# Optimization experiments

Hardware: AMD Instinct MI355X
Metric: run time of the kernel (lower is better)

## Reference

```python
import jax, jax.numpy as jnp
import numpy as np
import math


def setup_inputs() -> dict:
    key = jax.random.key(0)
    ks = jax.random.split(key, 8)
    B, S, dim = 4, 1024, 2048
    H, D = 16, 128          # n_heads = dim // core_dim
    T = 1024                # cached kv length
    w_scale = 1.0 / math.sqrt(dim)
    return {
        "x": jax.random.normal(ks[0], (B, S, dim), dtype=jnp.float32),
        "k_cache": jax.random.normal(ks[1], (B, H, T, D), dtype=jnp.float32),
        "v_cache": jax.random.normal(ks[2], (B, H, T, D), dtype=jnp.float32),
        "Wq": jax.random.normal(ks[3], (dim, dim), dtype=jnp.float32) * w_scale,
        "bq": jnp.zeros((dim,), jnp.float32),
        "Wk": jax.random.normal(ks[4], (dim, dim), dtype=jnp.float32) * w_scale,
        "bk": jnp.zeros((dim,), jnp.float32),
        "Wv": jax.random.normal(ks[5], (dim, dim), dtype=jnp.float32) * w_scale,
        "bv": jnp.zeros((dim,), jnp.float32),
        "Wo": jax.random.normal(ks[6], (dim, dim), dtype=jnp.float32) * w_scale,
        "bo": jnp.zeros((dim,), jnp.float32),
    }


def _split_heads(t, H):
    # [B, S, dim] -> [B, H, S, D]
    B, S, dim = t.shape
    return t.reshape(B, S, H, dim // H).transpose(0, 2, 1, 3)


def reference(x, k_cache, v_cache, Wq, bq, Wk, bk, Wv, bv, Wo, bo):
    B, S, dim = x.shape
    H = k_cache.shape[1]
    D = dim // H
    T = k_cache.shape[2]

    q = _split_heads(x @ Wq.T + bq, H)                 # [B,H,S,D]
    k_new = _split_heads(x @ Wk.T + bk, H)             # [B,H,S,D]
    v_new = _split_heads(x @ Wv.T + bv, H)

    k = jnp.concatenate([k_cache, k_new], axis=2)      # [B,H,T+S,D]
    v = jnp.concatenate([v_cache, v_new], axis=2)

    scale = 1.0 / math.sqrt(D)
    scores = jnp.einsum("bhqd,bhkd->bhqk", q, k) * scale   # [B,H,S,T+S]

    # causal mask with cache offset: query i may attend to key j iff j <= i + T
    q_pos = jnp.arange(S)[:, None] + T
    k_pos = jnp.arange(T + S)[None, :]
    mask = k_pos <= q_pos                              # [S, T+S]
    scores = jnp.where(mask[None, None], scores, jnp.finfo(scores.dtype).min)

    attn = jax.nn.softmax(scores, axis=-1)
    ctx = jnp.einsum("bhqk,bhkd->bhqd", attn, v)       # [B,H,S,D]
    ctx = ctx.transpose(0, 2, 1, 3).reshape(B, S, dim) # merge heads

    out = ctx @ Wo.T + bo                              # dropout is identity (p=0 / eval)
    return (out, k, v)
```

## Files before the change

kernel.cpp:

```cpp
#include <hip/hip_runtime.h>
#include <hip/hip_bf16.h>

typedef float f32x4 __attribute__((ext_vector_type(4)));
typedef __bf16 bf16x8 __attribute__((ext_vector_type(8)));
typedef unsigned short u16x8 __attribute__((ext_vector_type(8)));

#define DIMK 2048
#define QSCALE ((float)(0.08838834764831845 * 1.4426950408889634))

__device__ __forceinline__ unsigned short f2bf(float f) {
    union { float f; unsigned int u; } v; v.f = f;
    unsigned int r = v.u + 0x7fffu + ((v.u >> 16) & 1u);
    return (unsigned short)(r >> 16);
}
__device__ __forceinline__ float bf2f(unsigned short u) {
    union { unsigned int i; float f; } v; v.i = ((unsigned int)u) << 16; return v.f;
}

__device__ __forceinline__ void lds_load16(void* lds, const void* gsrc) {
    __builtin_amdgcn_global_load_lds(
        (const __attribute__((address_space(1))) unsigned int*)gsrc,
        (__attribute__((address_space(3))) unsigned int*)lds,
        16, 0, 0);
}

__global__ __launch_bounds__(256) void prep_all(
    const float* __restrict__ x,  const float* __restrict__ Wq,
    const float* __restrict__ Wk, const float* __restrict__ Wv,
    const float* __restrict__ Wo,
    const float* __restrict__ kc, const float* __restrict__ vc,
    unsigned short* __restrict__ xbf, unsigned short* __restrict__ Wqb,
    unsigned short* __restrict__ Wkb, unsigned short* __restrict__ Wvb,
    unsigned short* __restrict__ Wob,
    float* __restrict__ kout, unsigned short* __restrict__ Kbf,
    float* __restrict__ vout, unsigned short* __restrict__ Vtb)
{
    const int bid = blockIdx.x;
    const int tid = threadIdx.x;

    if (bid < 24576) {
        int i = bid * 256 + tid;
        const float* src; unsigned short* dst; size_t off;
        if (i < 2097152) { src = x; dst = xbf; off = i; }
        else {
            int j = (i - 2097152) >> 20;
            off = (size_t)((i - 2097152) & 1048575);
            src = j == 0 ? Wq : j == 1 ? Wk : j == 2 ? Wv : Wo;
            dst = j == 0 ? Wqb : j == 1 ? Wkb : j == 2 ? Wvb : Wob;
        }
        f32x4 v = *(const f32x4*)(src + off * 4);
        ushort4 pk = { f2bf(v[0]), f2bf(v[1]), f2bf(v[2]), f2bf(v[3]) };
        *(ushort4*)(dst + off * 4) = pk;
    } else if (bid < 32768) {
        size_t i4 = (size_t)(bid - 24576) * 256 + tid;
        size_t e = i4 * 4;
        size_t bh = e >> 17, rem = e & 131071;
        f32x4 v = *(const f32x4*)(kc + e);
        size_t dsto = (bh << 18) + rem;
        *(f32x4*)(kout + dsto) = v;
        ushort4 pk = { f2bf(v[0]), f2bf(v[1]), f2bf(v[2]), f2bf(v[3]) };
        *(ushort4*)(Kbf + dsto) = pk;
    } else {
        __shared__ unsigned short T[128 * 72];
        const int o = bid - 32768;
        const int kv0 = (o & 15) * 64;
        const int bh = o >> 4;
        const float* src = vc + ((size_t)bh << 17) + (size_t)kv0 * 128;
        float* vdst = vout + ((size_t)bh << 18) + (size_t)kv0 * 128;
        #pragma unroll
        for (int r = 0; r < 8; ++r) {
            int e4 = r * 256 + tid;
            int kv = e4 >> 5, d0 = (e4 & 31) << 2;
            f32x4 v = *(const f32x4*)(src + kv * 128 + d0);
            *(f32x4*)(vdst + kv * 128 + d0) = v;
            #pragma unroll
            for (int i = 0; i < 4; ++i) T[(d0 + i) * 72 + kv] = f2bf(v[i]);
        }
        __syncthreads();
        #pragma unroll
        for (int r = 0; r < 8; ++r) {
            int e = r * 256 + tid;
            int d = e >> 4, k4 = (e & 15) << 2;
            ushort4 pk = { T[d * 72 + k4], T[d * 72 + k4 + 1], T[d * 72 + k4 + 2], T[d * 72 + k4 + 3] };
            *(ushort4*)(Vtb + ((size_t)bh * 128 + d) * 2048 + kv0 + k4) = pk;
        }
    }
}

__device__ __forceinline__ void gemm_core(
    const unsigned short* __restrict__ A16, const unsigned short* __restrict__ W16,
    int m0, int n0, int tid, int w, int g, int c, int wr, int wc,
    unsigned short* As, unsigned short* Bs, f32x4 (&acc)[4][4])
{
    const int arow = tid >> 2;
    const int acol = (tid & 3) << 3;
    const unsigned short* Arow0 = A16 + (size_t)(m0 + arow) * DIMK + acol;
    const unsigned short* Arow1 = A16 + (size_t)(m0 + 64 + arow) * DIMK + acol;
    const unsigned short* Wrow0 = W16 + (size_t)(n0 + arow) * DIMK + acol;
    const unsigned short* Wrow1 = W16 + (size_t)(n0 + 64 + arow) * DIMK + acol;
    unsigned short* AsB0 = &As[(w * 64) * 8];
    unsigned short* AsB1 = &As[(256 + w * 64) * 8];
    unsigned short* BsB0 = &Bs[(w * 64) * 8];
    unsigned short* BsB1 = &Bs[(256 + w * 64) * 8];

    for (int k0 = 0; k0 < DIMK; k0 += 32) {
        __syncthreads();
        lds_load16(AsB0, Arow0 + k0);
        lds_load16(AsB1, Arow1 + k0);
        lds_load16(BsB0, Wrow0 + k0);
        lds_load16(BsB1, Wrow1 + k0);
        __syncthreads();

        bf16x8 af[4], bfr[4];
        #pragma unroll
        for (int i = 0; i < 4; ++i)
            af[i] = *(const bf16x8*)(&As[(wr * 64 + i * 16 + c) * 32 + g * 8]);
        #pragma unroll
        for (int i = 0; i < 4; ++i)
            bfr[i] = *(const bf16x8*)(&Bs[(wc * 64 + i * 16 + c) * 32 + g * 8]);
        #pragma unroll
        for (int i = 0; i < 4; ++i)
            #pragma unroll
            for (int j = 0; j < 4; ++j)
                acc[i][j] = __builtin_amdgcn_mfma_f32_16x16x32_bf16(af[i], bfr[j], acc[i][j], 0, 0, 0);
    }
}

__global__ __launch_bounds__(256) void gemm_qkv(
    const unsigned short* __restrict__ xbf,
    const unsigned short* __restrict__ Wqb, const unsigned short* __restrict__ Wkb,
    const unsigned short* __restrict__ Wvb,
    const float* __restrict__ bq, const float* __restrict__ bk, const float* __restrict__ bv,
    unsigned short* __restrict__ Qbf,
    float* __restrict__ kout, unsigned short* __restrict__ Kbf,
    float* __restrict__ vout, unsigned short* __restrict__ Vtb)
{
    const int o = blockIdx.x;
    const int xcd = o & 7;
    const int k = o >> 3;
    const int mblk = k & 31;
    const int nloc = k >> 5;
    const int nblk = xcd * 6 + nloc;
    const int m0 = mblk * 128;
    const int n0g = nblk * 128;
    const int mi = n0g >> 11;
    const int n0 = n0g & 2047;

    const unsigned short* W16 = mi == 0 ? Wqb : (mi == 1 ? Wkb : Wvb);
    const float* bias = mi == 0 ? bq : (mi == 1 ? bk : bv);

    const int tid = threadIdx.x;
    const int lane = tid & 63;
    const int w = tid >> 6;
    const int g = lane >> 4;
    const int c = lane & 15;
    const int wr = w >> 1, wc = w & 1;

    __shared__ unsigned short As[128 * 32];
    __shared__ unsigned short Bs[128 * 32];

    f32x4 acc[4][4];
    #pragma unroll
    for (int i = 0; i < 4; ++i)
        #pragma unroll
        for (int j = 0; j < 4; ++j)
            acc[i][j] = f32x4{0.f, 0.f, 0.f, 0.f};

    gemm_core(xbf, W16, m0, n0, tid, w, g, c, wr, wc, As, Bs, acc);

    #pragma unroll
    for (int j = 0; j < 4; ++j) {
        const int n = n0 + wc * 64 + j * 16 + c;
        const float bn = bias[n];
        const int hh = n >> 7, d = n & 127;
        #pragma unroll
        for (int i = 0; i < 4; ++i) {
            float y4[4];
            #pragma unroll
            for (int tq = 0; tq < 4; ++tq) y4[tq] = acc[i][j][tq] + bn;
            const int mb = m0 + wr * 64 + i * 16 + g * 4;
            if (mi == 0) {
                #pragma unroll
                for (int tq = 0; tq < 4; ++tq) {
                    int m = mb + tq; int b = m >> 10, s = m & 1023;
                    Qbf[((((size_t)b * 16 + hh) << 10) + s) * 128 + d] = f2bf(y4[tq] * QSCALE);
                }
            } else if (mi == 1) {
                #pragma unroll
                for (int tq = 0; tq < 4; ++tq) {
                    int m = mb + tq; int b = m >> 10, s = m & 1023;
                    kout[(((size_t)b * 16 + hh) * 2048 + 1024 + s) * 128 + d] = y4[tq];
                    Kbf[(((size_t)b * 16 + hh) << 18) + (size_t)(1024 + s) * 128 + d] = f2bf(y4[tq]);
                }
            } else {
                #pragma unroll
                for (int tq = 0; tq < 4; ++tq) {
                    int m = mb + tq; int b = m >> 10, s = m & 1023;
                    vout[(((size_t)b * 16 + hh) * 2048 + 1024 + s) * 128 + d] = y4[tq];
                }
                int b = mb >> 10, s = mb & 1023;
                ushort4 pk = { f2bf(y4[0]), f2bf(y4[1]), f2bf(y4[2]), f2bf(y4[3]) };
                *(ushort4*)(Vtb + (((size_t)b * 16 + hh) * 128 + d) * 2048 + 1024 + s) = pk;
            }
        }
    }
}

__global__ __launch_bounds__(256) void gemm_wo(
    const unsigned short* __restrict__ ctx, const unsigned short* __restrict__ Wob,
    const float* __restrict__ bo, float* __restrict__ outp)
{
    const int o = blockIdx.x;
    const int xcd = o & 7;
    const int k = o >> 3;
    const int mblk = k & 31;
    const int nloc = k >> 5;
    const int nblk = xcd * 2 + nloc;
    const int m0 = mblk * 128;
    const int n0 = nblk * 128;

    const int tid = threadIdx.x;
    const int lane = tid & 63;
    const int w = tid >> 6;
    const int g = lane >> 4;
    const int c = lane & 15;
    const int wr = w >> 1, wc = w & 1;

    __shared__ unsigned short As[128 * 32];
    __shared__ unsigned short Bs[128 * 32];

    f32x4 acc[4][4];
    #pragma unroll
    for (int i = 0; i < 4; ++i)
        #pragma unroll
        for (int j = 0; j < 4; ++j)
            acc[i][j] = f32x4{0.f, 0.f, 0.f, 0.f};

    gemm_core(ctx, Wob, m0, n0, tid, w, g, c, wr, wc, As, Bs, acc);

    #pragma unroll
    for (int j = 0; j < 4; ++j) {
        const int n = n0 + wc * 64 + j * 16 + c;
        const float bn = bo[n];
        #pragma unroll
        for (int i = 0; i < 4; ++i) {
            const int mb = m0 + wr * 64 + i * 16 + g * 4;
            #pragma unroll
            for (int tq = 0; tq < 4; ++tq)
                outp[(size_t)(mb + tq) * 2048 + n] = acc[i][j][tq] + bn;
        }
    }
}

__global__ __launch_bounds__(256) void attn8(
    const unsigned short* __restrict__ Qbf,
    const unsigned short* __restrict__ Kbf,
    const unsigned short* __restrict__ Vtb,
    unsigned short* __restrict__ Pp,
    float* __restrict__ Mp,
    float* __restrict__ Lp)
{
    const int o = blockIdx.x;
    const int xcd = o & 7;
    const int kk0 = o >> 3;
    const int half = kk0 & 1;
    const int qt = 7 - ((kk0 >> 1) & 7);
    const int bh = (kk0 >> 4) * 8 + xcd;

    const int tid = threadIdx.x;
    const int lane = tid & 63;
    const int w = tid >> 6;
    const int g = lane >> 4;
    const int c = lane & 15;
    const int cswz = (c & 7) << 3;

    __shared__ unsigned short Ks[2][64 * 128];
    __shared__ unsigned short Vs[128 * 64];

    const unsigned short* Qb = Qbf + ((size_t)bh * 1024 + qt * 128) * 128;
    const unsigned short* Kb = Kbf + ((size_t)bh << 18);
    const unsigned short* Vt = Vtb + ((size_t)bh << 18);

    bf16x8 aq[2][4];
    #pragma unroll
    for (int m2 = 0; m2 < 2; ++m2)
        #pragma unroll
        for (int kd = 0; kd < 4; ++kd)
            aq[m2][kd] = *(const bf16x8*)(Qb + (w * 32 + m2 * 16 + c) * 128 + kd * 32 + g * 8);

    f32x4 od[2][8];
    #pragma unroll
    for (int m2 = 0; m2 < 2; ++m2)
        #pragma unroll
        for (int nf = 0; nf < 8; ++nf)
            od[m2][nf] = f32x4{0.f, 0.f, 0.f, 0.f};
    float mrow[2] = { -1e30f, -1e30f };
    float lrow[2] = { 0.f, 0.f };

    const int krow = tid >> 4;
    const int kswz = (((tid & 15) << 4) ^ ((krow & 7) << 4)) >> 1;
    const unsigned short* Kl = Kb + (size_t)krow * 128 + kswz;

    const int vd = tid >> 3;
    const int ck = tid & 7;
    const int kkv = ck >> 2;
    const int av = (ck >> 1) & 1;
    const int p0 = kkv * 32 + (((2 * ck) & 3) << 3) + av * 4;
    const int p1 = kkv * 32 + (((2 * ck + 1) & 3) << 3) + av * 4;

    const int cnt = 9 + qt;
    const int t0 = half * cnt;
    const int lim_min = 1024 + qt * 128 + w * 32;

    u16x8 vreg0, vreg1, vreg2, vreg3;

    {
        const int kv0 = t0 * 64;
        #pragma unroll
        for (int r = 0; r < 4; ++r)
            lds_load16(&Ks[0][w * 512 + r * 2048], Kl + (size_t)(kv0 + r * 16) * 128);
        vreg0 = *(const u16x8*)(Vt + (size_t)(vd +  0) * 2048 + kv0 + ck * 8);
        vreg1 = *(const u16x8*)(Vt + (size_t)(vd + 32) * 2048 + kv0 + ck * 8);
        vreg2 = *(const u16x8*)(Vt + (size_t)(vd + 64) * 2048 + kv0 + ck * 8);
        vreg3 = *(const u16x8*)(Vt + (size_t)(vd + 96) * 2048 + kv0 + ck * 8);
        #pragma unroll
        for (int r = 0; r < 4; ++r) {
            const int d = vd + r * 32;
            const int sw = (d & 7) << 3;
            unsigned short* row = &Vs[d * 64];
            u16x8 vv = r == 0 ? vreg0 : r == 1 ? vreg1 : r == 2 ? vreg2 : vreg3;
            ushort4 lo = { vv[0], vv[1], vv[2], vv[3] };
            ushort4 hi = { vv[4], vv[5], vv[6], vv[7] };
            *(ushort4*)(&row[p0 ^ sw]) = lo;
            *(ushort4*)(&row[p1 ^ sw]) = hi;
        }
        __syncthreads();
    }

    int cur = 0;
    for (int t = t0; t < t0 + cnt; ++t) {
        const int kv0 = t * 64;
        const bool next = (t + 1 < t0 + cnt);

        if (next) {
            const int kvn = kv0 + 64;
            #pragma unroll
            for (int r = 0; r < 4; ++r)
                lds_load16(&Ks[cur ^ 1][w * 512 + r * 2048], Kl + (size_t)(kvn + r * 16) * 128);
            vreg0 = *(const u16x8*)(Vt + (size_t)(vd +  0) * 2048 + kvn + ck * 8);
            vreg1 = *(const u16x8*)(Vt + (size_t)(vd + 32) * 2048 + kvn + ck * 8);
            vreg2 = *(const u16x8*)(Vt + (size_t)(vd + 64) * 2048 + kvn + ck * 8);
            vreg3 = *(const u16x8*)(Vt + (size_t)(vd + 96) * 2048 + kvn + ck * 8);
        }

        const unsigned short* Ksc = &Ks[cur][0];

        f32x4 sc[2][4];
        #pragma unroll
        for (int m2 = 0; m2 < 2; ++m2)
            #pragma unroll
            for (int n = 0; n < 4; ++n)
                sc[m2][n] = f32x4{0.f, 0.f, 0.f, 0.f};
        #pragma unroll
        for (int kd = 0; kd < 4; ++kd) {
            bf16x8 bk[4];
            #pragma unroll
            for (int n = 0; n < 4; ++n)
                bk[n] = *(const bf16x8*)(&Ksc[(n * 16 + c) * 128 + ((kd * 32 + g * 8) ^ cswz)]);
            #pragma unroll
            for (int m2 = 0; m2 < 2; ++m2)
                #pragma unroll
                for (int n = 0; n < 4; ++n)
                    sc[m2][n] = __builtin_amdgcn_mfma_f32_16x16x32_bf16(bk[n], aq[m2][kd], sc[m2][n], 0, 0, 0);
        }

        const bool need_mask = (kv0 + 63 > lim_min);
        #pragma unroll
        for (int m2 = 0; m2 < 2; ++m2) {
            if (need_mask) {
                const int lim = lim_min + m2 * 16 + c;
                #pragma unroll
                for (int n = 0; n < 4; ++n)
                    #pragma unroll
                    for (int j = 0; j < 4; ++j)
                        if (kv0 + n * 16 + g * 4 + j > lim) sc[m2][n][j] = -1e30f;
            }
            float t4[4];
            #pragma unroll
            for (int n = 0; n < 4; ++n)
                t4[n] = fmaxf(fmaxf(sc[m2][n][0], sc[m2][n][1]),
                              fmaxf(sc[m2][n][2], sc[m2][n][3]));
            float rmax = fmaxf(fmaxf(t4[0], t4[1]), fmaxf(t4[2], t4[3]));
            rmax = fmaxf(rmax, __shfl_xor(rmax, 16));
            rmax = fmaxf(rmax, __shfl_xor(rmax, 32));

            if (!__all(rmax <= mrow[m2] + 8.0f)) {
                const float mnew = fmaxf(mrow[m2], rmax);
                const float fs = exp2f(mrow[m2] - mnew);
                mrow[m2] = mnew;
                lrow[m2] *= fs;
                #pragma unroll
                for (int j = 0; j < 4; ++j) {
                    const float fsj = __shfl(fs, (lane & 48) | (g * 4 + j));
                    #pragma unroll
                    for (int nf = 0; nf < 8; ++nf)
                        od[m2][nf][j] *= fsj;
                }
            }
            const float mm = mrow[m2];
            float s4[4];
            #pragma unroll
            for (int n = 0; n < 4; ++n) {
                #pragma unroll
                for (int j = 0; j < 4; ++j) {
                    float p = exp2f(sc[m2][n][j] - mm);
                    sc[m2][n][j] = p;
                }
                s4[n] = (sc[m2][n][0] + sc[m2][n][1]) + (sc[m2][n][2] + sc[m2][n][3]);
            }
            float rsum = (s4[0] + s4[1]) + (s4[2] + s4[3]);
            rsum += __shfl_xor(rsum, 16);
            rsum += __shfl_xor(rsum, 32);
            lrow[m2] += rsum;
        }

        bf16x8 pa[2][2];
        #pragma unroll
        for (int m2 = 0; m2 < 2; ++m2)
            #pragma unroll
            for (int kk = 0; kk < 2; ++kk)
                #pragma unroll
                for (int e = 0; e < 8; ++e)
                    pa[m2][kk][e] = (__bf16)sc[m2][2 * kk + (e >> 2)][e & 3];

        #pragma unroll
        for (int kk = 0; kk < 2; ++kk) {
            #pragma unroll
            for (int nf = 0; nf < 8; ++nf) {
                bf16x8 bv = *(const bf16x8*)(&Vs[(nf * 16 + c) * 64 + ((kk * 32 + g * 8) ^ cswz)]);
                od[0][nf] = __builtin_amdgcn_mfma_f32_16x16x32_bf16(pa[0][kk], bv, od[0][nf], 0, 0, 0);
                od[1][nf] = __builtin_amdgcn_mfma_f32_16x16x32_bf16(pa[1][kk], bv, od[1][nf], 0, 0, 0);
            }
        }

        __syncthreads();

        if (next) {
            #pragma unroll
            for (int r = 0; r < 4; ++r) {
                const int d = vd + r * 32;
                const int sw = (d & 7) << 3;
                unsigned short* row = &Vs[d * 64];
                u16x8 vv = r == 0 ? vreg0 : r == 1 ? vreg1 : r == 2 ? vreg2 : vreg3;
                ushort4 lo = { vv[0], vv[1], vv[2], vv[3] };
                ushort4 hi = { vv[4], vv[5], vv[6], vv[7] };
                *(ushort4*)(&row[p0 ^ sw]) = lo;
                *(ushort4*)(&row[p1 ^ sw]) = hi;
            }
        }

        __syncthreads();
        cur ^= 1;
    }

    const size_t pbase = ((size_t)(half * 64 + bh) * 1024 + qt * 128) * 128;
    const int mlbase = (half * 64 + bh) * 1024 + qt * 128;
    if (lane < 16) {
        #pragma unroll
        for (int m2 = 0; m2 < 2; ++m2) {
            Mp[mlbase + w * 32 + m2 * 16 + c] = mrow[m2];
            Lp[mlbase + w * 32 + m2 * 16 + c] = lrow[m2];
        }
    }
    #pragma unroll
    for (int m2 = 0; m2 < 2; ++m2) {
        #pragma unroll
        for (int j = 0; j < 4; ++j) {
            const float lj = __shfl(lrow[m2], (lane & 48) | (g * 4 + j));
            const float rl = 1.0f / lj;
            const int ql = w * 32 + m2 * 16 + g * 4 + j;
            #pragma unroll
            for (int nf = 0; nf < 8; ++nf)
                Pp[pbase + (size_t)ql * 128 + nf * 16 + c] = f2bf(od[m2][nf][j] * rl);
        }
    }
}

__global__ __launch_bounds__(256) void merge_ctx(
    const unsigned short* __restrict__ Pp, const float* __restrict__ Mp,
    const float* __restrict__ Lp, unsigned short* __restrict__ ctx)
{
    const int idx = blockIdx.x * 256 + threadIdx.x;
    const int r = idx >> 4;
    const int dc = (idx & 15) << 3;
    const float m0 = Mp[r], m1 = Mp[65536 + r];
    const float l0 = Lp[r], l1 = Lp[65536 + r];
    const float M = fmaxf(m0, m1);
    float w0 = l0 * exp2f(m0 - M);
    float w1 = l1 * exp2f(m1 - M);
    const float inv = 1.0f / (w0 + w1);
    w0 *= inv; w1 *= inv;
    u16x8 a = *(const u16x8*)(Pp + (size_t)r * 128 + dc);
    u16x8 bb = *(const u16x8*)(Pp + (size_t)8388608 + (size_t)r * 128 + dc);
    const int bh = r >> 10, q = r & 1023;
    unsigned short* dst = ctx + ((size_t)(bh >> 4) * 1024 + q) * 2048 + (bh & 15) * 128 + dc;
    u16x8 outv;
    #pragma unroll
    for (int e = 0; e < 8; ++e)
        outv[e] = f2bf(w0 * bf2f(a[e]) + w1 * bf2f(bb[e]));
    *(u16x8*)dst = outv;
}

__global__ __launch_bounds__(256) void copy_cache(
    const float* __restrict__ kc, const float* __restrict__ vc,
    float* __restrict__ kout, float* __restrict__ vout)
{
    size_t i4 = (size_t)blockIdx.x * 256 + threadIdx.x;
    const float* src = blockIdx.y ? vc : kc;
    float* dst = blockIdx.y ? vout : kout;
    size_t e = i4 * 4;
    size_t bh = e >> 17, rem = e & 131071;
    f32x4 v = *(const f32x4*)(src + e);
    *(f32x4*)(dst + (bh << 18) + rem) = v;
}

template<int MODE, bool ABF16>
__global__ __launch_bounds__(256) void gemm_bt(
    const void* __restrict__ Ag, const float* __restrict__ Wf,
    const float* __restrict__ bias, void* __restrict__ dst)
{
    const int tid = threadIdx.x;
    const int lane = tid & 63;
    const int w = tid >> 6;
    const int g = lane >> 4;
    const int c = lane & 15;
    const int wr = w >> 1, wc = w & 1;
    const int m0 = blockIdx.y * 128;
    const int n0 = blockIdx.x * 128;

    __shared__ unsigned short As[128 * 40];
    __shared__ unsigned short Bs[128 * 40];

    f32x4 acc[4][4];
    #pragma unroll
    for (int i = 0; i < 4; ++i)
        #pragma unroll
        for (int j = 0; j < 4; ++j)
            acc[i][j] = f32x4{0.f, 0.f, 0.f, 0.f};

    for (int k0 = 0; k0 < DIMK; k0 += 32) {
        __syncthreads();
        if constexpr (ABF16) {
            const unsigned short* A16 = (const unsigned short*)Ag;
            #pragma unroll
            for (int r = 0; r < 2; ++r) {
                int e8 = r * 256 + tid;
                int row = e8 >> 2, col = (e8 & 3) << 3;
                *(uint4*)(&As[row * 40 + col]) =
                    *(const uint4*)(A16 + (size_t)(m0 + row) * DIMK + k0 + col);
            }
        } else {
            const float* Af = (const float*)Ag;
            #pragma unroll
            for (int r = 0; r < 4; ++r) {
                int e4 = r * 256 + tid;
                int row = e4 >> 3, col = (e4 & 7) << 2;
                f32x4 v = *(const f32x4*)(Af + (size_t)(m0 + row) * DIMK + k0 + col);
                ushort4 pk = { f2bf(v[0]), f2bf(v[1]), f2bf(v[2]), f2bf(v[3]) };
                *(ushort4*)(&As[row * 40 + col]) = pk;
            }
        }
        {
            #pragma unroll
            for (int r = 0; r < 4; ++r) {
                int e4 = r * 256 + tid;
                int row = e4 >> 3, col = (e4 & 7) << 2;
                f32x4 v = *(const f32x4*)(Wf + (size_t)(n0 + row) * DIMK + k0 + col);
                ushort4 pk = { f2bf(v[0]), f2bf(v[1]), f2bf(v[2]), f2bf(v[3]) };
                *(ushort4*)(&Bs[row * 40 + col]) = pk;
            }
        }
        __syncthreads();

        bf16x8 af[4], bfr[4];
        #pragma unroll
        for (int i = 0; i < 4; ++i)
            af[i] = *(const bf16x8*)(&As[(wr * 64 + i * 16 + c) * 40 + g * 8]);
        #pragma unroll
        for (int i = 0; i < 4; ++i)
            bfr[i] = *(const bf16x8*)(&Bs[(wc * 64 + i * 16 + c) * 40 + g * 8]);
        #pragma unroll
        for (int i = 0; i < 4; ++i)
            #pragma unroll
            for (int j = 0; j < 4; ++j)
                acc[i][j] = __builtin_amdgcn_mfma_f32_16x16x32_bf16(af[i], bfr[j], acc[i][j], 0, 0, 0);
    }

    #pragma unroll
    for (int j = 0; j < 4; ++j) {
        const int n = n0 + wc * 64 + j * 16 + c;
        const float bn = bias[n];
        #pragma unroll
        for (int i = 0; i < 4; ++i) {
            float y4[4];
            #pragma unroll
            for (int tq = 0; tq < 4; ++tq) y4[tq] = acc[i][j][tq] + bn;
            const int mb = m0 + wr * 64 + i * 16 + g * 4;
            if constexpr (MODE == 0) {
                #pragma unroll
                for (int tq = 0; tq < 4; ++tq) {
                    int m = mb + tq; int b = m >> 10, s = m & 1023;
                    int hh = n >> 7, d = n & 127;
                    ((unsigned short*)dst)[((((size_t)b * 16 + hh) << 10) + s) * 128 + d] = f2bf(y4[tq] * QSCALE);
                }
            } else if constexpr (MODE == 1) {
                #pragma unroll
                for (int tq = 0; tq < 4; ++tq) {
                    int m = mb + tq; int b = m >> 10, s = m & 1023;
                    int hh = n >> 7, d = n & 127;
                    ((float*)dst)[(((size_t)b * 16 + hh) * 2048 + 1024 + s) * 128 + d] = y4[tq];
                }
            } else {
                #pragma unroll
                for (int tq = 0; tq < 4; ++tq)
                    ((float*)dst)[(size_t)(mb + tq) * 2048 + n] = y4[tq];
            }
        }
    }
}

__global__ __launch_bounds__(256) void attn_stage(
    const unsigned short* __restrict__ Qbf,
    const float* __restrict__ Kf, const float* __restrict__ Vf,
    unsigned short* __restrict__ ctx)
{
    const int qt = blockIdx.x;
    const int bh = blockIdx.y;
    const int b = bh >> 4, h = bh & 15;
    const int tid = threadIdx.x;
    const int lane = tid & 63;
    const int w = tid >> 6;
    const int g = lane >> 4;
    const int c = lane & 15;

    __shared__ unsigned short Ksl[64 * 136];
    __shared__ unsigned short Vtl[128 * 72];
    __shared__ unsigned short Ps[4 * 32 * 72];

    bf16x8 aq[2][4];
    const unsigned short* Qb = Qbf + ((size_t)bh * 1024 + qt * 128) * 128;
    #pragma unroll
    for (int m2 = 0; m2 < 2; ++m2)
        #pragma unroll
        for (int kk = 0; kk < 4; ++kk)
            aq[m2][kk] = *(const bf16x8*)(Qb + (w * 32 + m2 * 16 + c) * 128 + kk * 32 + g * 8);

    f32x4 od[2][8];
    #pragma unroll
    for (int m2 = 0; m2 < 2; ++m2)
        #pragma unroll
        for (int nf = 0; nf < 8; ++nf)
            od[m2][nf] = f32x4{0.f, 0.f, 0.f, 0.f};
    float mrow[2][4], lrow[2][4];
    #pragma unroll
    for (int m2 = 0; m2 < 2; ++m2)
        #pragma unroll
        for (int j = 0; j < 4; ++j) { mrow[m2][j] = -1e30f; lrow[m2][j] = 0.f; }

    const float* Kb = Kf + (size_t)bh * 2048 * 128;
    const float* Vb = Vf + (size_t)bh * 2048 * 128;
    const int ntiles = 18 + 2 * qt;

    for (int t = 0; t < ntiles; ++t) {
        __syncthreads();
        const float* Kt = Kb + (size_t)t * 64 * 128;
        #pragma unroll
        for (int r = 0; r < 8; ++r) {
            int e4 = r * 256 + tid;
            int kv = e4 >> 5, d0 = (e4 & 31) << 2;
            f32x4 v = *(const f32x4*)(Kt + kv * 128 + d0);
            ushort4 pk = { f2bf(v[0]), f2bf(v[1]), f2bf(v[2]), f2bf(v[3]) };
            *(ushort4*)(&Ksl[kv * 136 + d0]) = pk;
        }
        const float* Vg = Vb + (size_t)t * 64 * 128;
        #pragma unroll
        for (int r = 0; r < 8; ++r) {
            int e4 = tid * 8 + r;
            int kv = e4 >> 5, d0 = (e4 & 31) << 2;
            f32x4 v = *(const f32x4*)(Vg + kv * 128 + d0);
            #pragma unroll
            for (int i = 0; i < 4; ++i)
                Vtl[(d0 + i) * 72 + kv] = f2bf(v[i]);
        }
        __syncthreads();

        f32x4 sc[2][4];
        #pragma unroll
        for (int m2 = 0; m2 < 2; ++m2)
            #pragma unroll
            for (int n = 0; n < 4; ++n)
                sc[m2][n] = f32x4{0.f, 0.f, 0.f, 0.f};
        #pragma unroll
        for (int kk = 0; kk < 4; ++kk) {
            bf16x8 bk[4];
            #pragma unroll
            for (int n = 0; n < 4; ++n)
                bk[n] = *(const bf16x8*)(&Ksl[(n * 16 + c) * 136 + kk * 32 + g * 8]);
            #pragma unroll
            for (int m2 = 0; m2 < 2; ++m2)
                #pragma unroll
                for (int n = 0; n < 4; ++n)
                    sc[m2][n] = __builtin_amdgcn_mfma_f32_16x16x32_bf16(aq[m2][kk], bk[n], sc[m2][n], 0, 0, 0);
        }

        const int kvbase = t * 64;
        #pragma unroll
        for (int m2 = 0; m2 < 2; ++m2) {
            #pragma unroll
            for (int j = 0; j < 4; ++j) {
                const int qg = qt * 128 + w * 32 + m2 * 16 + g * 4 + j;
                const int lim = qg + 1024;
                float rmax = -1e30f;
                #pragma unroll
                for (int n = 0; n < 4; ++n) {
                    float s = sc[m2][n][j] * QSCALE;
                    if (kvbase + n * 16 + c > lim) s = -1e30f;
                    sc[m2][n][j] = s;
                    rmax = fmaxf(rmax, s);
                }
                #pragma unroll
                for (int off = 1; off < 16; off <<= 1)
                    rmax = fmaxf(rmax, __shfl_xor(rmax, off));
                float mold = mrow[m2][j];
                float mnew = fmaxf(mold, rmax);
                mrow[m2][j] = mnew;
                float fs = exp2f(mold - mnew);
                float rsum = 0.f;
                #pragma unroll
                for (int n = 0; n < 4; ++n) {
                    float p = exp2f(sc[m2][n][j] - mnew);
                    sc[m2][n][j] = p;
                    rsum += p;
                }
                #pragma unroll
                for (int off = 1; off < 16; off <<= 1)
                    rsum += __shfl_xor(rsum, off);
                lrow[m2][j] = lrow[m2][j] * fs + rsum;
                #pragma unroll
                for (int nf = 0; nf < 8; ++nf)
                    od[m2][nf][j] *= fs;
            }
        }

        unsigned short* Pw = &Ps[w * 32 * 72];
        #pragma unroll
        for (int m2 = 0; m2 < 2; ++m2)
            #pragma unroll
            for (int n = 0; n < 4; ++n)
                #pragma unroll
                for (int j = 0; j < 4; ++j)
                    Pw[(m2 * 16 + g * 4 + j) * 72 + n * 16 + c] = f2bf(sc[m2][n][j]);

        #pragma unroll
        for (int kk = 0; kk < 2; ++kk) {
            bf16x8 ap0 = *(const bf16x8*)(&Ps[(w * 32 + c) * 72 + kk * 32 + g * 8]);
            bf16x8 ap1 = *(const bf16x8*)(&Ps[(w * 32 + 16 + c) * 72 + kk * 32 + g * 8]);
            #pragma unroll
            for (int nf = 0; nf < 8; ++nf) {
                bf16x8 bv = *(const bf16x8*)(&Vtl[(nf * 16 + c) * 72 + kk * 32 + g * 8]);
                od[0][nf] = __builtin_amdgcn_mfma_f32_16x16x32_bf16(ap0, bv, od[0][nf], 0, 0, 0);
                od[1][nf] = __builtin_amdgcn_mfma_f32_16x16x32_bf16(ap1, bv, od[1][nf], 0, 0, 0);
            }
        }
    }

    #pragma unroll
    for (int m2 = 0; m2 < 2; ++m2) {
        #pragma unroll
        for (int j = 0; j < 4; ++j) {
            const int qg = qt * 128 + w * 32 + m2 * 16 + g * 4 + j;
            const float rl = 1.0f / lrow[m2][j];
            #pragma unroll
            for (int nf = 0; nf < 8; ++nf) {
                const int d = nf * 16 + c;
                ctx[((size_t)b * 1024 + qg) * 2048 + h * 128 + d] = f2bf(od[m2][nf][j] * rl);
            }
        }
    }
}

extern "C" void kernel_launch(void* const* d_in, const int* in_sizes, int n_in,
                              void* d_out, int out_size, void* d_ws, size_t ws_size,
                              hipStream_t stream) {
    const float* x  = (const float*)d_in[0];
    const float* kc = (const float*)d_in[1];
    const float* vc = (const float*)d_in[2];
    const float* Wq = (const float*)d_in[3];
    const float* bq = (const float*)d_in[4];
    const float* Wk = (const float*)d_in[5];
    const float* bk = (const float*)d_in[6];
    const float* Wv = (const float*)d_in[7];
    const float* bv = (const float*)d_in[8];
    const float* Wo = (const float*)d_in[9];
    const float* bo = (const float*)d_in[10];

    float* outp = (float*)d_out;
    float* kout = outp + (size_t)8388608;
    float* vout = outp + (size_t)25165824;

    unsigned short* Qbf = (unsigned short*)d_ws;
    unsigned short* ctx = Qbf + (size_t)8388608;
    unsigned short* Kbf = ctx + (size_t)8388608;
    unsigned short* Vtb = Kbf + (size_t)16777216;
    unsigned short* xbf = Vtb + (size_t)16777216;
    unsigned short* Wqb = xbf + (size_t)8388608;
    unsigned short* Wkb = Wqb + (size_t)4194304;
    unsigned short* Wvb = Wkb + (size_t)4194304;
    unsigned short* Wob = Wvb + (size_t)4194304;
    unsigned short* Pp = xbf;
    float* Mp = (float*)Wvb;
    float* Lp = Mp + (size_t)131072;

    const bool full = ws_size >= (size_t)150994944;

    if (full) {
        prep_all<<<33792, 256, 0, stream>>>(x, Wq, Wk, Wv, Wo, kc, vc,
                                            xbf, Wqb, Wkb, Wvb, Wob,
                                            kout, Kbf, vout, Vtb);
        gemm_qkv<<<1536, 256, 0, stream>>>(xbf, Wqb, Wkb, Wvb, bq, bk, bv,
                                           Qbf, kout, Kbf, vout, Vtb);
        attn8<<<1024, 256, 0, stream>>>(Qbf, Kbf, Vtb, Pp, Mp, Lp);
        merge_ctx<<<4096, 256, 0, stream>>>(Pp, Mp, Lp, ctx);
        gemm_wo<<<512, 256, 0, stream>>>(ctx, Wob, bo, outp);
    } else {
        copy_cache<<<dim3(8192, 2), 256, 0, stream>>>(kc, vc, kout, vout);
        gemm_bt<0, false><<<dim3(16, 32), 256, 0, stream>>>(x, Wq, bq, Qbf);
        gemm_bt<1, false><<<dim3(16, 32), 256, 0, stream>>>(x, Wk, bk, kout);
        gemm_bt<1, false><<<dim3(16, 32), 256, 0, stream>>>(x, Wv, bv, vout);
        attn_stage<<<dim3(8, 64), 256, 0, stream>>>(Qbf, kout, vout, ctx);
        gemm_bt<2, true><<<dim3(16, 32), 256, 0, stream>>>(ctx, Wo, bo, outp);
    }
}
```

Before: 435.4 us.

## Pre-tile and pre-swizzle V^T so attention loads it directly into LDS with 8 waves

The producers of V^T (prep_all and gemm_qkv) now write it as 64-key tiles that already carry the LDS permutation and XOR swizzle. The attention kernel can then copy V into a double-buffered LDS tile with global_load_lds instead of staging it through registers and scattered LDS writes. The attention kernel also moves from 4 waves with 32 query rows each to 8 waves with 16 rows each (512 threads). This halves per-wave accumulator register use and should raise latency hiding, but it doubles the LDS spent on V buffers and reuses each K/V fragment read for fewer query rows.

```diff
diff --git a/kernel.cpp b/kernel.cpp
--- a/kernel.cpp
+++ b/kernel.cpp
@@ -22,6 +22,10 @@
         (const __attribute__((address_space(1))) unsigned int*)gsrc,
         (__attribute__((address_space(3))) unsigned int*)lds,
         16, 0, 0);
+}
+
+__device__ __forceinline__ int vperm4(int kv4) {
+    return ((kv4 >> 5) << 5) + (((kv4 >> 2) & 3) << 3) + (((kv4 >> 4) & 1) << 2);
 }
 
 __global__ __launch_bounds__(256) void prep_all(
@@ -33,7 +37,7 @@
     unsigned short* __restrict__ Wkb, unsigned short* __restrict__ Wvb,
     unsigned short* __restrict__ Wob,
     float* __restrict__ kout, unsigned short* __restrict__ Kbf,
-    float* __restrict__ vout, unsigned short* __restrict__ Vtb)
+    float* __restrict__ vout, unsigned short* __restrict__ Vtp)
 {
     const int bid = blockIdx.x;
     const int tid = threadIdx.x;
@@ -63,7 +67,8 @@
     } else {
         __shared__ unsigned short T[128 * 72];
         const int o = bid - 32768;
-        const int kv0 = (o & 15) * 64;
+        const int t = o & 15;
+        const int kv0 = t * 64;
         const int bh = o >> 4;
         const float* src = vc + ((size_t)bh << 17) + (size_t)kv0 * 128;
         float* vdst = vout + ((size_t)bh << 18) + (size_t)kv0 * 128;
@@ -77,12 +82,14 @@
             for (int i = 0; i < 4; ++i) T[(d0 + i) * 72 + kv] = f2bf(v[i]);
         }
         __syncthreads();
+        unsigned short* tile = Vtp + ((size_t)bh * 32 + t) * 8192;
         #pragma unroll
         for (int r = 0; r < 8; ++r) {
             int e = r * 256 + tid;
             int d = e >> 4, k4 = (e & 15) << 2;
             ushort4 pk = { T[d * 72 + k4], T[d * 72 + k4 + 1], T[d * 72 + k4 + 2], T[d * 72 + k4 + 3] };
-            *(ushort4*)(Vtb + ((size_t)bh * 128 + d) * 2048 + kv0 + k4) = pk;
+            const int idx = d * 64 + (vperm4(k4) ^ ((d & 7) << 3));
+            *(ushort4*)(tile + idx) = pk;
         }
     }
 }
@@ -133,7 +140,7 @@
     const float* __restrict__ bq, const float* __restrict__ bk, const float* __restrict__ bv,
     unsigned short* __restrict__ Qbf,
     float* __restrict__ kout, unsigned short* __restrict__ Kbf,
-    float* __restrict__ vout, unsigned short* __restrict__ Vtb)
+    float* __restrict__ vout, unsigned short* __restrict__ Vtp)
 {
     const int o = blockIdx.x;
     const int xcd = o & 7;
@@ -199,8 +206,10 @@
                     vout[(((size_t)b * 16 + hh) * 2048 + 1024 + s) * 128 + d] = y4[tq];
                 }
                 int b = mb >> 10, s = mb & 1023;
+                const int t = 16 + (s >> 6);
+                const int idx = d * 64 + (vperm4(s & 63) ^ ((d & 7) << 3));
                 ushort4 pk = { f2bf(y4[0]), f2bf(y4[1]), f2bf(y4[2]), f2bf(y4[3]) };
-                *(ushort4*)(Vtb + (((size_t)b * 16 + hh) * 128 + d) * 2048 + 1024 + s) = pk;
+                *(ushort4*)(Vtp + ((size_t)(b * 16 + hh) * 32 + t) * 8192 + idx) = pk;
             }
         }
     }
@@ -252,10 +261,10 @@
     }
 }
 
-__global__ __launch_bounds__(256) void attn8(
+__global__ __launch_bounds__(512) void attn9(
     const unsigned short* __restrict__ Qbf,
     const unsigned short* __restrict__ Kbf,
-    const unsigned short* __restrict__ Vtb,
+    const unsigned short* __restrict__ Vtp,
     unsigned short* __restrict__ Pp,
     float* __restrict__ Mp,
     float* __restrict__ Lp)
@@ -275,65 +284,38 @@
     const int cswz = (c & 7) << 3;
 
     __shared__ unsigned short Ks[2][64 * 128];
-    __shared__ unsigned short Vs[128 * 64];
+    __shared__ unsigned short Vs[2][64 * 128];
 
     const unsigned short* Qb = Qbf + ((size_t)bh * 1024 + qt * 128) * 128;
     const unsigned short* Kb = Kbf + ((size_t)bh << 18);
-    const unsigned short* Vt = Vtb + ((size_t)bh << 18);
-
-    bf16x8 aq[2][4];
-    #pragma unroll
-    for (int m2 = 0; m2 < 2; ++m2)
-        #pragma unroll
-        for (int kd = 0; kd < 4; ++kd)
-            aq[m2][kd] = *(const bf16x8*)(Qb + (w * 32 + m2 * 16 + c) * 128 + kd * 32 + g * 8);
-
-    f32x4 od[2][8];
-    #pragma unroll
-    for (int m2 = 0; m2 < 2; ++m2)
-        #pragma unroll
-        for (int nf = 0; nf < 8; ++nf)
-            od[m2][nf] = f32x4{0.f, 0.f, 0.f, 0.f};
-    float mrow[2] = { -1e30f, -1e30f };
-    float lrow[2] = { 0.f, 0.f };
+    const unsigned short* Vtile = Vtp + (size_t)bh * 32 * 8192;
+
+    bf16x8 aq[4];
+    #pragma unroll
+    for (int kd = 0; kd < 4; ++kd)
+        aq[kd] = *(const bf16x8*)(Qb + (w * 16 + c) * 128 + kd * 32 + g * 8);
+
+    f32x4 od[8];
+    #pragma unroll
+    for (int nf = 0; nf < 8; ++nf)
+        od[nf] = f32x4{0.f, 0.f, 0.f, 0.f};
+    float mrow = -1e30f, lrow = 0.f;
 
     const int krow = tid >> 4;
     const int kswz = (((tid & 15) << 4) ^ ((krow & 7) << 4)) >> 1;
     const unsigned short* Kl = Kb + (size_t)krow * 128 + kswz;
 
-    const int vd = tid >> 3;
-    const int ck = tid & 7;
-    const int kkv = ck >> 2;
-    const int av = (ck >> 1) & 1;
-    const int p0 = kkv * 32 + (((2 * ck) & 3) << 3) + av * 4;
-    const int p1 = kkv * 32 + (((2 * ck + 1) & 3) << 3) + av * 4;
-
     const int cnt = 9 + qt;
     const int t0 = half * cnt;
-    const int lim_min = 1024 + qt * 128 + w * 32;
-
-    u16x8 vreg0, vreg1, vreg2, vreg3;
+    const int limw = 1024 + qt * 128 + w * 16;
 
     {
         const int kv0 = t0 * 64;
-        #pragma unroll
-        for (int r = 0; r < 4; ++r)
-            lds_load16(&Ks[0][w * 512 + r * 2048], Kl + (size_t)(kv0 + r * 16) * 128);
-        vreg0 = *(const u16x8*)(Vt + (size_t)(vd +  0) * 2048 + kv0 + ck * 8);
-        vreg1 = *(const u16x8*)(Vt + (size_t)(vd + 32) * 2048 + kv0 + ck * 8);
-        vreg2 = *(const u16x8*)(Vt + (size_t)(vd + 64) * 2048 + kv0 + ck * 8);
-        vreg3 = *(const u16x8*)(Vt + (size_t)(vd + 96) * 2048 + kv0 + ck * 8);
-        #pragma unroll
-        for (int r = 0; r < 4; ++r) {
-            const int d = vd + r * 32;
-            const int sw = (d & 7) << 3;
-            unsigned short* row = &Vs[d * 64];
-            u16x8 vv = r == 0 ? vreg0 : r == 1 ? vreg1 : r == 2 ? vreg2 : vreg3;
-            ushort4 lo = { vv[0], vv[1], vv[2], vv[3] };
-            ushort4 hi = { vv[4], vv[5], vv[6], vv[7] };
-            *(ushort4*)(&row[p0 ^ sw]) = lo;
-            *(ushort4*)(&row[p1 ^ sw]) = hi;
-        }
+        lds_load16(&Ks[0][w * 512], Kl + (size_t)kv0 * 128);
+        lds_load16(&Ks[0][4096 + w * 512], Kl + (size_t)(kv0 + 32) * 128);
+        const unsigned short* Vsrc = Vtile + (size_t)t0 * 8192 + tid * 8;
+        lds_load16(&Vs[0][w * 512], Vsrc);
+        lds_load16(&Vs[0][4096 + w * 512], Vsrc + 4096);
         __syncthreads();
     }
 
@@ -344,23 +326,20 @@
 
         if (next) {
             const int kvn = kv0 + 64;
-            #pragma unroll
-            for (int r = 0; r < 4; ++r)
-                lds_load16(&Ks[cur ^ 1][w * 512 + r * 2048], Kl + (size_t)(kvn + r * 16) * 128);
-            vreg0 = *(const u16x8*)(Vt + (size_t)(vd +  0) * 2048 + kvn + ck * 8);
-            vreg1 = *(const u16x8*)(Vt + (size_t)(vd + 32) * 2048 + kvn + ck * 8);
-            vreg2 = *(const u16x8*)(Vt + (size_t)(vd + 64) * 2048 + kvn + ck * 8);
-            vreg3 = *(const u16x8*)(Vt + (size_t)(vd + 96) * 2048 + kvn + ck * 8);
+            lds_load16(&Ks[cur ^ 1][w * 512], Kl + (size_t)kvn * 128);
+            lds_load16(&Ks[cur ^ 1][4096 + w * 512], Kl + (size_t)(kvn + 32) * 128);
+            const unsigned short* Vsrc = Vtile + (size_t)(t + 1) * 8192 + tid * 8;
+            lds_load16(&Vs[cur ^ 1][w * 512], Vsrc);
+            lds_load16(&Vs[cur ^ 1][4096 + w * 512], Vsrc + 4096);
         }
 
         const unsigned short* Ksc = &Ks[cur][0];
-
-        f32x4 sc[2][4];
-        #pragma unroll
-        for (int m2 = 0; m2 < 2; ++m2)
-            #pragma unroll
-            for (int n = 0; n < 4; ++n)
-                sc[m2][n] = f32x4{0.f, 0.f, 0.f, 0.f};
+        const unsigned short* Vsc = &Vs[cur][0];
+
+        f32x4 sc[4];
+        #pragma unroll
+        for (int n = 0; n < 4; ++n)
+            sc[n] = f32x4{0.f, 0.f, 0.f, 0.f};
         #pragma unroll
         for (int kd = 0; kd < 4; ++kd) {
             bf16x8 bk[4];
@@ -368,94 +347,69 @@
             for (int n = 0; n < 4; ++n)
                 bk[n] = *(const bf16x8*)(&Ksc[(n * 16 + c) * 128 + ((kd * 32 + g * 8) ^ cswz)]);
             #pragma unroll
-            for (int m2 = 0; m2 < 2; ++m2)
-                #pragma unroll
-                for (int n = 0; n < 4; ++n)
-                    sc[m2][n] = __builtin_amdgcn_mfma_f32_16x16x32_bf16(bk[n], aq[m2][kd], sc[m2][n], 0, 0, 0);
-        }
-
-        const bool need_mask = (kv0 + 63 > lim_min);
-        #pragma unroll
-        for (int m2 = 0; m2 < 2; ++m2) {
-            if (need_mask) {
-                const int lim = lim_min + m2 * 16 + c;
-                #pragma unroll
-                for (int n = 0; n < 4; ++n)
-                    #pragma unroll
-                    for (int j = 0; j < 4; ++j)
-                        if (kv0 + n * 16 + g * 4 + j > lim) sc[m2][n][j] = -1e30f;
-            }
+            for (int n = 0; n < 4; ++n)
+                sc[n] = __builtin_amdgcn_mfma_f32_16x16x32_bf16(bk[n], aq[kd], sc[n], 0, 0, 0);
+        }
+
+        const bool need_mask = (kv0 + 63 > limw);
+        if (need_mask) {
+            const int lim = limw + c;
+            #pragma unroll
+            for (int n = 0; n < 4; ++n)
+                #pragma unroll
+                for (int j = 0; j < 4; ++j)
+                    if (kv0 + n * 16 + g * 4 + j > lim) sc[n][j] = -1e30f;
+        }
+        {
             float t4[4];
             #pragma unroll
             for (int n = 0; n < 4; ++n)
-                t4[n] = fmaxf(fmaxf(sc[m2][n][0], sc[m2][n][1]),
-                              fmaxf(sc[m2][n][2], sc[m2][n][3]));
+                t4[n] = fmaxf(fmaxf(sc[n][0], sc[n][1]), fmaxf(sc[n][2], sc[n][3]));
             float rmax = fmaxf(fmaxf(t4[0], t4[1]), fmaxf(t4[2], t4[3]));
             rmax = fmaxf(rmax, __shfl_xor(rmax, 16));
             rmax = fmaxf(rmax, __shfl_xor(rmax, 32));
 
-            if (!__all(rmax <= mrow[m2] + 8.0f)) {
-                const float mnew = fmaxf(mrow[m2], rmax);
-                const float fs = exp2f(mrow[m2] - mnew);
-                mrow[m2] = mnew;
-                lrow[m2] *= fs;
+            if (!__all(rmax <= mrow + 8.0f)) {
+                const float mnew = fmaxf(mrow, rmax);
+                const float fs = exp2f(mrow - mnew);
+                mrow = mnew;
+                lrow *= fs;
                 #pragma unroll
                 for (int j = 0; j < 4; ++j) {
                     const float fsj = __shfl(fs, (lane & 48) | (g * 4 + j));
                     #pragma unroll
                     for (int nf = 0; nf < 8; ++nf)
-                        od[m2][nf][j] *= fsj;
+                        od[nf][j] *= fsj;
                 }
             }
-            const float mm = mrow[m2];
+            const float mm = mrow;
             float s4[4];
             #pragma unroll
             for (int n = 0; n < 4; ++n) {
                 #pragma unroll
-                for (int j = 0; j < 4; ++j) {
-                    float p = exp2f(sc[m2][n][j] - mm);
-                    sc[m2][n][j] = p;
-                }
-                s4[n] = (sc[m2][n][0] + sc[m2][n][1]) + (sc[m2][n][2] + sc[m2][n][3]);
+                for (int j = 0; j < 4; ++j)
+                    sc[n][j] = exp2f(sc[n][j] - mm);
+                s4[n] = (sc[n][0] + sc[n][1]) + (sc[n][2] + sc[n][3]);
             }
             float rsum = (s4[0] + s4[1]) + (s4[2] + s4[3]);
             rsum += __shfl_xor(rsum, 16);
             rsum += __shfl_xor(rsum, 32);
-            lrow[m2] += rsum;
-        }
-
-        bf16x8 pa[2][2];
-        #pragma unroll
-        for (int m2 = 0; m2 < 2; ++m2)
-            #pragma unroll
-            for (int kk = 0; kk < 2; ++kk)
-                #pragma unroll
-                for (int e = 0; e < 8; ++e)
-                    pa[m2][kk][e] = (__bf16)sc[m2][2 * kk + (e >> 2)][e & 3];
+            lrow += rsum;
+        }
+
+        bf16x8 pa[2];
+        #pragma unroll
+        for (int kk = 0; kk < 2; ++kk)
+            #pragma unroll
+            for (int e = 0; e < 8; ++e)
+                pa[kk][e] = (__bf16)sc[2 * kk + (e >> 2)][e & 3];
 
         #pragma unroll
         for (int kk = 0; kk < 2; ++kk) {
             #pragma unroll
             for (int nf = 0; nf < 8; ++nf) {
-                bf16x8 bv = *(const bf16x8*)(&Vs[(nf * 16 + c) * 64 + ((kk * 32 + g * 8) ^ cswz)]);
-                od[0][nf] = __builtin_amdgcn_mfma_f32_16x16x32_bf16(pa[0][kk], bv, od[0][nf], 0, 0, 0);
-                od[1][nf] = __builtin_amdgcn_mfma_f32_16x16x32_bf16(pa[1][kk], bv, od[1][nf], 0, 0, 0);
-            }
-        }
-
-        __syncthreads();
-
-        if (next) {
-            #pragma unroll
-            for (int r = 0; r < 4; ++r) {
-                const int d = vd + r * 32;
-                const int sw = (d & 7) << 3;
-                unsigned short* row = &Vs[d * 64];
-                u16x8 vv = r == 0 ? vreg0 : r == 1 ? vreg1 : r == 2 ? vreg2 : vreg3;
-                ushort4 lo = { vv[0], vv[1], vv[2], vv[3] };
-                ushort4 hi = { vv[4], vv[5], vv[6], vv[7] };
-                *(ushort4*)(&row[p0 ^ sw]) = lo;
-                *(ushort4*)(&row[p1 ^ sw]) = hi;
+                bf16x8 bv = *(const bf16x8*)(&Vsc[(nf * 16 + c) * 64 + ((kk * 32 + g * 8) ^ cswz)]);
+                od[nf] = __builtin_amdgcn_mfma_f32_16x16x32_bf16(pa[kk], bv, od[nf], 0, 0, 0);
             }
         }
 
@@ -466,23 +420,17 @@
     const size_t pbase = ((size_t)(half * 64 + bh) * 1024 + qt * 128) * 128;
     const int mlbase = (half * 64 + bh) * 1024 + qt * 128;
     if (lane < 16) {
-        #pragma unroll
-        for (int m2 = 0; m2 < 2; ++m2) {
-            Mp[mlbase + w * 32 + m2 * 16 + c] = mrow[m2];
-            Lp[mlbase + w * 32 + m2 * 16 + c] = lrow[m2];
-        }
-    }
-    #pragma unroll
-    for (int m2 = 0; m2 < 2; ++m2) {
-        #pragma unroll
-        for (int j = 0; j < 4; ++j) {
-            const float lj = __shfl(lrow[m2], (lane & 48) | (g * 4 + j));
-            const float rl = 1.0f / lj;
-            const int ql = w * 32 + m2 * 16 + g * 4 + j;
-            #pragma unroll
-            for (int nf = 0; nf < 8; ++nf)
-                Pp[pbase + (size_t)ql * 128 + nf * 16 + c] = f2bf(od[m2][nf][j] * rl);
-        }
+        Mp[mlbase + w * 16 + c] = mrow;
+        Lp[mlbase + w * 16 + c] = lrow;
+    }
+    #pragma unroll
+    for (int j = 0; j < 4; ++j) {
+        const float lj = __shfl(lrow, (lane & 48) | (g * 4 + j));
+        const float rl = 1.0f / lj;
+        const int ql = w * 16 + g * 4 + j;
+        #pragma unroll
+        for (int nf = 0; nf < 8; ++nf)
+            Pp[pbase + (size_t)ql * 128 + nf * 16 + c] = f2bf(od[nf][j] * rl);
     }
 }
 
@@ -811,8 +759,8 @@
     unsigned short* Qbf = (unsigned short*)d_ws;
     unsigned short* ctx = Qbf + (size_t)8388608;
     unsigned short* Kbf = ctx + (size_t)8388608;
-    unsigned short* Vtb = Kbf + (size_t)16777216;
-    unsigned short* xbf = Vtb + (size_t)16777216;
+    unsigned short* Vtp = Kbf + (size_t)16777216;
+    unsigned short* xbf = Vtp + (size_t)16777216;
     unsigned short* Wqb = xbf + (size_t)8388608;
     unsigned short* Wkb = Wqb + (size_t)4194304;
     unsigned short* Wvb = Wkb + (size_t)4194304;
@@ -826,10 +774,10 @@
     if (full) {
         prep_all<<<33792, 256, 0, stream>>>(x, Wq, Wk, Wv, Wo, kc, vc,
                                             xbf, Wqb, Wkb, Wvb, Wob,
-                                            kout, Kbf, vout, Vtb);
+                                            kout, Kbf, vout, Vtp);
         gemm_qkv<<<1536, 256, 0, stream>>>(xbf, Wqb, Wkb, Wvb, bq, bk, bv,
-                                           Qbf, kout, Kbf, vout, Vtb);
-        attn8<<<1024, 256, 0, stream>>>(Qbf, Kbf, Vtb, Pp, Mp, Lp);
+                                           Qbf, kout, Kbf, vout, Vtp);
+        attn9<<<1024, 512, 0, stream>>>(Qbf, Kbf, Vtp, Pp, Mp, Lp);
         merge_ctx<<<4096, 256, 0, stream>>>(Pp, Mp, Lp, ctx);
         gemm_wo<<<512, 256, 0, stream>>>(ctx, Wob, bo, outp);
     } else {
```

New measurement: 378.4 us. -13.1%, faster.
